# Optimization experiments

Measured on AMD Instinct MI355X. Metric: run time of the kernel, lower is better.

Reference implementation:

```python
import jax, jax.numpy as jnp
import numpy as np

CODE_DIM = 256
HIDDEN = 128
HEADS = 4
N_CODES = 100000
N_SPEC = 256


def setup_inputs() -> dict:
    key = jax.random.key(0)
    ks = jax.random.split(key, 7)
    provider_emb = jax.random.normal(ks[0], (CODE_DIM,), jnp.float32)
    code_embs = jax.random.normal(ks[1], (N_CODES, CODE_DIM), jnp.float32)
    # per-head Linear(code_dim -> hidden): stacked weights [H, D, K] and bias [H, K]
    W = jax.random.normal(ks[2], (HEADS, CODE_DIM, HIDDEN), jnp.float32) / np.sqrt(CODE_DIM)
    b = jax.random.normal(ks[3], (HEADS, HIDDEN), jnp.float32) * 0.01
    # attention vectors a: [H, 2*hidden] (squeezed trailing 1)
    a = jax.random.normal(ks[4], (HEADS, 2 * HIDDEN), jnp.float32) * 0.01
    # classifier Linear(hidden*heads -> num_specialties)
    Wc = jax.random.normal(ks[5], (N_SPEC, HIDDEN * HEADS), jnp.float32) / np.sqrt(HIDDEN * HEADS)
    bc = jax.random.normal(ks[6], (N_SPEC,), jnp.float32) * 0.01
    return {"provider_emb": provider_emb, "code_embs": code_embs,
            "W": W, "b": b, "a": a, "Wc": Wc, "bc": bc}


def reference(provider_emb, code_embs, W, b, a, Wc, bc):
    # provider projection per head: [H, K]
    provider_h = jnp.einsum('d,hdk->hk', provider_emb, W) + b
    # code projection per head: [H, N, K]
    code_h = jnp.einsum('nd,hdk->hnk', code_embs, W) + b[:, None, :]
    a1, a2 = a[:, :HIDDEN], a[:, HIDDEN:]           # split concat attention vec
    # e[h,n] = leaky_relu(provider_h[h].a1[h] + code_h[h,n].a2[h])
    e = jnp.einsum('hk,hk->h', provider_h, a1)[:, None] \
        + jnp.einsum('hnk,hk->hn', code_h, a2)
    e = jnp.where(e >= 0, e, 0.2 * e)               # LeakyReLU(0.2)
    alpha = jax.nn.softmax(e, axis=1)               # softmax over code nodes
    # dropout is identity in eval mode
    agg = jnp.einsum('hn,hnk->hk', alpha, code_h)   # weighted sum per head
    multi_head_output = agg.reshape(-1)             # [H*K]
    specialty_logits = multi_head_output @ Wc.T + bc
    return specialty_logits, multi_head_output
```

## Files before the change

kernel.cpp:

```cpp
#include <hip/hip_runtime.h>
#include <hip/hip_bf16.h>

#define CODE_DIM 256
#define HIDDEN   128
#define HEADS    4
#define N_CODES  100000
#define N_SPEC   256

#define K2_BLOCKS 1024
#define K2_TPB    256
#define K2_WPB    4
#define K2_WAVES  (K2_BLOCKS * K2_WPB)
#define WROWS     8
#define NTILES    (N_CODES / WROWS)
#define RSTRIDE   260
#define NSLOTS    64

#define WS_V       0
#define WS_CP      1024
#define WS_SLOT    1040
#define SLOT_STRIDE 1028

#define LDS_VSH   0
#define LDS_TSH   1024
#define LDS_TILE  1152
#define LDS_TOTAL (LDS_TILE + K2_WPB * WROWS * RSTRIDE)

#define WAITCNT_VM0   0x0F70
#define WAITCNT_LGKM0 0xC07F

typedef __attribute__((address_space(1))) const void* as1cv;
typedef __attribute__((address_space(3))) void*       as3v;

__global__ void k1_prep(const float* __restrict__ pe, const float* __restrict__ W,
                        const float* __restrict__ b, const float* __restrict__ a,
                        float* __restrict__ ws) {
    const int bx = blockIdx.x;
    const int h = bx >> 2, dq = bx & 3;
    const int tid = threadIdx.x;
    const int dl = tid >> 2, q = tid & 3;
    const int d = dq * 64 + dl;
    __shared__ float a_sh[2 * HIDDEN];
    __shared__ float cred[4];
    a_sh[tid] = a[h * 2 * HIDDEN + tid];
    __syncthreads();

    const float4* wr = (const float4*)(W + ((size_t)(h * CODE_DIM + d)) * HIDDEN + q * 32);
    float u = 0.f, v = 0.f;
#pragma unroll
    for (int j = 0; j < 8; ++j) {
        float4 wv = wr[j];
        int k = q * 32 + j * 4;
        u += wv.x * a_sh[k]     + wv.y * a_sh[k + 1]
           + wv.z * a_sh[k + 2] + wv.w * a_sh[k + 3];
        v += wv.x * a_sh[HIDDEN + k]     + wv.y * a_sh[HIDDEN + k + 1]
           + wv.z * a_sh[HIDDEN + k + 2] + wv.w * a_sh[HIDDEN + k + 3];
    }
    u += __shfl_xor(u, 1, 64); u += __shfl_xor(u, 2, 64);
    v += __shfl_xor(v, 1, 64); v += __shfl_xor(v, 2, 64);
    if (q == 0) ws[WS_V + h * CODE_DIM + d] = v;

    float cp = (q == 0) ? pe[d] * u : 0.f;
    if (dq == 0 && tid < HIDDEN) cp += b[h * HIDDEN + tid] * (a_sh[tid] + a_sh[HIDDEN + tid]);
#pragma unroll
    for (int off = 32; off; off >>= 1) cp += __shfl_xor(cp, off, 64);
    if ((tid & 63) == 0) cred[tid >> 6] = cp;
    __syncthreads();
    if (tid == 0) ws[WS_CP + h * 4 + dq] = cred[0] + cred[1] + cred[2] + cred[3];

    float4* z = (float4*)(ws + WS_SLOT);
    const int g = bx * 256 + tid;
#pragma unroll
    for (int i = 0; i < 5; ++i) {
        int idx = g + i * 4096;
        if (idx < (NSLOTS * SLOT_STRIDE) / 4) z[idx] = make_float4(0.f, 0.f, 0.f, 0.f);
    }
}

__global__ __launch_bounds__(K2_TPB, 4) void k2_main(const float* __restrict__ code,
                                                     float* __restrict__ ws) {
    __shared__ float lds[LDS_TOTAL];
    const int tid  = threadIdx.x;
    const int lane = tid & 63;
    const int w    = tid >> 6;
    const int row  = lane >> 3;
    const int seg  = lane & 7;
    const int bx   = blockIdx.x;

    {
        float4 vv = ((const float4*)(ws + WS_V))[tid];
        *(float4*)&lds[LDS_VSH + tid * 4] = vv;
    }
    float ch[HEADS];
#pragma unroll
    for (int h = 0; h < HEADS; ++h) {
        float4 cc = *(const float4*)(ws + WS_CP + 4 * h);
        ch[h] = cc.x + cc.y + cc.z + cc.w;
    }
    __syncthreads();

    const int tilebase = LDS_TILE + w * (WROWS * RSTRIDE);
    const int xb = tilebase + row * RSTRIDE + seg * 32;

    float4 acc0 = make_float4(0,0,0,0), acc1 = acc0, acc2 = acc0, acc3 = acc0;
    float ds0 = 0.f, ds1 = 0.f, ds2 = 0.f, ds3 = 0.f;

    for (int tile = bx * K2_WPB + w; tile < NTILES; tile += K2_WAVES) {
        __builtin_amdgcn_s_waitcnt(WAITCNT_LGKM0);
        const float* gbase = code + (size_t)tile * (WROWS * CODE_DIM) + lane * 4;
#pragma unroll
        for (int r = 0; r < WROWS; ++r) {
            __builtin_amdgcn_global_load_lds((as1cv)(gbase + r * CODE_DIM),
                                             (as3v)&lds[tilebase + r * RSTRIDE], 16, 0, 0);
        }
        __builtin_amdgcn_s_waitcnt(WAITCNT_VM0);

        float p0 = 0.f, p1 = 0.f, p2 = 0.f, p3 = 0.f;
#pragma unroll
        for (int c = 0; c < 8; ++c) {
            float4 x4 = *(const float4*)&lds[xb + c * 4];
            float4 va = *(const float4*)&lds[LDS_VSH +   0 + seg * 32 + c * 4];
            float4 vb = *(const float4*)&lds[LDS_VSH + 256 + seg * 32 + c * 4];
            float4 vc = *(const float4*)&lds[LDS_VSH + 512 + seg * 32 + c * 4];
            float4 vd = *(const float4*)&lds[LDS_VSH + 768 + seg * 32 + c * 4];
            p0 += x4.x * va.x + x4.y * va.y + x4.z * va.z + x4.w * va.w;
            p1 += x4.x * vb.x + x4.y * vb.y + x4.z * vb.z + x4.w * vb.w;
            p2 += x4.x * vc.x + x4.y * vc.y + x4.z * vc.z + x4.w * vc.w;
            p3 += x4.x * vd.x + x4.y * vd.y + x4.z * vd.z + x4.w * vd.w;
        }
#pragma unroll
        for (int off = 1; off < 8; off <<= 1) {
            p0 += __shfl_xor(p0, off, 64);
            p1 += __shfl_xor(p1, off, 64);
            p2 += __shfl_xor(p2, off, 64);
            p3 += __shfl_xor(p3, off, 64);
        }
        float e0 = p0 + ch[0]; e0 = (e0 >= 0.f) ? e0 : 0.2f * e0; float t0 = __expf(e0);
        float e1 = p1 + ch[1]; e1 = (e1 >= 0.f) ? e1 : 0.2f * e1; float t1 = __expf(e1);
        float e2 = p2 + ch[2]; e2 = (e2 >= 0.f) ? e2 : 0.2f * e2; float t2 = __expf(e2);
        float e3 = p3 + ch[3]; e3 = (e3 >= 0.f) ? e3 : 0.2f * e3; float t3 = __expf(e3);
        ds0 += t0; ds1 += t1; ds2 += t2; ds3 += t3;
        if (seg == 0) *(float4*)&lds[LDS_TSH + w * 32 + row * 4] = make_float4(t0, t1, t2, t3);
        __builtin_amdgcn_s_waitcnt(WAITCNT_LGKM0);

#pragma unroll
        for (int r = 0; r < WROWS; ++r) {
            float4 tr = *(const float4*)&lds[LDS_TSH + w * 32 + r * 4];
            float4 x4 = *(const float4*)&lds[tilebase + r * RSTRIDE + lane * 4];
            acc0.x += tr.x * x4.x; acc0.y += tr.x * x4.y; acc0.z += tr.x * x4.z; acc0.w += tr.x * x4.w;
            acc1.x += tr.y * x4.x; acc1.y += tr.y * x4.y; acc1.z += tr.y * x4.z; acc1.w += tr.y * x4.w;
            acc2.x += tr.z * x4.x; acc2.y += tr.z * x4.y; acc2.z += tr.z * x4.z; acc2.w += tr.z * x4.w;
            acc3.x += tr.w * x4.x; acc3.y += tr.w * x4.y; acc3.z += tr.w * x4.z; acc3.w += tr.w * x4.w;
        }
    }

    __syncthreads();
    *(float4*)&lds[w * 1024 +   0 + 4 * lane] = acc0;
    *(float4*)&lds[w * 1024 + 256 + 4 * lane] = acc1;
    *(float4*)&lds[w * 1024 + 512 + 4 * lane] = acc2;
    *(float4*)&lds[w * 1024 + 768 + 4 * lane] = acc3;
    *(float4*)&lds[4096 + (w * 64 + lane) * 4] = make_float4(ds0, ds1, ds2, ds3);
    __syncthreads();

    float* slot = ws + WS_SLOT + (size_t)(bx & (NSLOTS - 1)) * SLOT_STRIDE;
    for (int o = tid; o < HEADS * CODE_DIM; o += K2_TPB) {
        float s = lds[o] + lds[1024 + o] + lds[2048 + o] + lds[3072 + o];
        atomicAdd(slot + o, s);
    }
    {
        const int h = tid >> 6, l2 = tid & 63;
        float dv = lds[4096 +   0 + l2 * 4 + h] + lds[4096 + 256 + l2 * 4 + h]
                 + lds[4096 + 512 + l2 * 4 + h] + lds[4096 + 768 + l2 * 4 + h];
#pragma unroll
        for (int off = 32; off; off >>= 1) dv += __shfl_xor(dv, off, 64);
        if (l2 == 0) atomicAdd(slot + HEADS * CODE_DIM + h, dv * 0.125f);
    }
}

__global__ void k3_agg(const float* __restrict__ W, const float* __restrict__ b,
                       const float* __restrict__ ws, float* __restrict__ out) {
    const int bx = blockIdx.x;
    const int h = bx >> 2, q = bx & 3;
    const int tid = threadIdx.x;
    __shared__ float s_sh[CODE_DIM];
    __shared__ float yred[8 * 32];
    __shared__ float den_sh;
    const float* slots = ws + WS_SLOT;

    if (tid < 64) {
        float dv = slots[(size_t)tid * SLOT_STRIDE + HEADS * CODE_DIM + h];
#pragma unroll
        for (int off = 32; off; off >>= 1) dv += __shfl_xor(dv, off, 64);
        if (tid == 0) den_sh = dv;
    }
    float su = 0.f;
#pragma unroll 8
    for (int s2 = 0; s2 < NSLOTS; ++s2)
        su += slots[(size_t)s2 * SLOT_STRIDE + h * CODE_DIM + tid];
    __syncthreads();
    s_sh[tid] = su / den_sh;
    __syncthreads();

    const int c = tid >> 5, kl = tid & 31;
    float y = 0.f;
    const float* wp = W + ((size_t)(h * CODE_DIM + c * 32)) * HIDDEN + q * 32 + kl;
#pragma unroll 8
    for (int d = 0; d < 32; ++d) y += s_sh[c * 32 + d] * wp[(size_t)d * HIDDEN];
    yred[c * 32 + kl] = y;
    __syncthreads();
    if (tid < 32) {
        float t = 0.f;
#pragma unroll
        for (int cc = 0; cc < 8; ++cc) t += yred[cc * 32 + tid];
        out[N_SPEC + h * HIDDEN + q * 32 + tid] = t + b[h * HIDDEN + q * 32 + tid];
    }
}

__global__ void k4_logits(const float* __restrict__ Wc, const float* __restrict__ bc,
                          float* __restrict__ out) {
    const int lane = threadIdx.x & 63;
    const int wv   = threadIdx.x >> 6;
    const int i    = blockIdx.x * 4 + wv;
    const float4* wr  = (const float4*)(Wc + (size_t)i * (HEADS * HIDDEN));
    const float4* mh4 = (const float4*)(out + N_SPEC);
    float4 wa = wr[lane],      ma = mh4[lane];
    float4 wb = wr[64 + lane], mb = mh4[64 + lane];
    float pp = wa.x * ma.x + wa.y * ma.y + wa.z * ma.z + wa.w * ma.w
             + wb.x * mb.x + wb.y * mb.y + wb.z * mb.z + wb.w * mb.w;
#pragma unroll
    for (int off = 32; off; off >>= 1) pp += __shfl_xor(pp, off, 64);
    if (lane == 0) out[i] = pp + bc[i];
}

extern "C" void kernel_launch(void* const* d_in, const int* in_sizes, int n_in,
                              void* d_out, int out_size, void* d_ws, size_t ws_size,
                              hipStream_t stream) {
    const float* pe   = (const float*)d_in[0];
    const float* code = (const float*)d_in[1];
    const float* W    = (const float*)d_in[2];
    const float* b    = (const float*)d_in[3];
    const float* a    = (const float*)d_in[4];
    const float* Wc   = (const float*)d_in[5];
    const float* bc   = (const float*)d_in[6];
    float* out = (float*)d_out;
    float* ws  = (float*)d_ws;

    k1_prep<<<16, 256, 0, stream>>>(pe, W, b, a, ws);
    k2_main<<<K2_BLOCKS, K2_TPB, 0, stream>>>(code, ws);
    k3_agg<<<16, 256, 0, stream>>>(W, b, ws, out);
    k4_logits<<<64, 256, 0, stream>>>(Wc, bc, out);
}
```

Measured before the change: 177.9 us.

## Use atomic work-stealing tile counter in main kernel and widen prep grid

Result: slower. 334.0 us (+87.7%).

```diff
diff --git a/kernel.cpp b/kernel.cpp
--- a/kernel.cpp
+++ b/kernel.cpp
@@ -10,7 +10,6 @@
 #define K2_BLOCKS 1024
 #define K2_TPB    256
 #define K2_WPB    4
-#define K2_WAVES  (K2_BLOCKS * K2_WPB)
 #define WROWS     8
 #define NTILES    (N_CODES / WROWS)
 #define RSTRIDE   260
@@ -18,7 +17,8 @@
 
 #define WS_V       0
 #define WS_CP      1024
-#define WS_SLOT    1040
+#define WS_CTR     1088
+#define WS_SLOT    1104
 #define SLOT_STRIDE 1028
 
 #define LDS_VSH   0
@@ -36,50 +36,54 @@
                         const float* __restrict__ b, const float* __restrict__ a,
                         float* __restrict__ ws) {
     const int bx = blockIdx.x;
-    const int h = bx >> 2, dq = bx & 3;
+    const int h = bx >> 4, dseg = bx & 15;
     const int tid = threadIdx.x;
-    const int dl = tid >> 2, q = tid & 3;
-    const int d = dq * 64 + dl;
+    const int dl = tid >> 4;
+    const int q  = tid & 15;
+    const int d  = dseg * 16 + dl;
     __shared__ float a_sh[2 * HIDDEN];
     __shared__ float cred[4];
     a_sh[tid] = a[h * 2 * HIDDEN + tid];
     __syncthreads();
 
-    const float4* wr = (const float4*)(W + ((size_t)(h * CODE_DIM + d)) * HIDDEN + q * 32);
+    const float4* wr = (const float4*)(W + ((size_t)(h * CODE_DIM + d)) * HIDDEN + q * 8);
     float u = 0.f, v = 0.f;
 #pragma unroll
-    for (int j = 0; j < 8; ++j) {
+    for (int j = 0; j < 2; ++j) {
         float4 wv = wr[j];
-        int k = q * 32 + j * 4;
+        int k = q * 8 + j * 4;
         u += wv.x * a_sh[k]     + wv.y * a_sh[k + 1]
            + wv.z * a_sh[k + 2] + wv.w * a_sh[k + 3];
         v += wv.x * a_sh[HIDDEN + k]     + wv.y * a_sh[HIDDEN + k + 1]
            + wv.z * a_sh[HIDDEN + k + 2] + wv.w * a_sh[HIDDEN + k + 3];
     }
-    u += __shfl_xor(u, 1, 64); u += __shfl_xor(u, 2, 64);
-    v += __shfl_xor(v, 1, 64); v += __shfl_xor(v, 2, 64);
+#pragma unroll
+    for (int off = 1; off < 16; off <<= 1) {
+        u += __shfl_xor(u, off, 64);
+        v += __shfl_xor(v, off, 64);
+    }
     if (q == 0) ws[WS_V + h * CODE_DIM + d] = v;
 
     float cp = (q == 0) ? pe[d] * u : 0.f;
-    if (dq == 0 && tid < HIDDEN) cp += b[h * HIDDEN + tid] * (a_sh[tid] + a_sh[HIDDEN + tid]);
+    if (dseg == 0 && tid < HIDDEN) cp += b[h * HIDDEN + tid] * (a_sh[tid] + a_sh[HIDDEN + tid]);
 #pragma unroll
     for (int off = 32; off; off >>= 1) cp += __shfl_xor(cp, off, 64);
     if ((tid & 63) == 0) cred[tid >> 6] = cp;
     __syncthreads();
-    if (tid == 0) ws[WS_CP + h * 4 + dq] = cred[0] + cred[1] + cred[2] + cred[3];
+    if (tid == 0) ws[WS_CP + bx] = cred[0] + cred[1] + cred[2] + cred[3];
+    if (bx == 0 && tid == 0) *(int*)(ws + WS_CTR) = 0;
 
     float4* z = (float4*)(ws + WS_SLOT);
     const int g = bx * 256 + tid;
-#pragma unroll
-    for (int i = 0; i < 5; ++i) {
-        int idx = g + i * 4096;
-        if (idx < (NSLOTS * SLOT_STRIDE) / 4) z[idx] = make_float4(0.f, 0.f, 0.f, 0.f);
-    }
+    const int nz = (NSLOTS * SLOT_STRIDE) / 4;
+    z[g] = make_float4(0.f, 0.f, 0.f, 0.f);
+    if (g + 16384 < nz) z[g + 16384] = make_float4(0.f, 0.f, 0.f, 0.f);
 }
 
 __global__ __launch_bounds__(K2_TPB, 4) void k2_main(const float* __restrict__ code,
                                                      float* __restrict__ ws) {
     __shared__ float lds[LDS_TOTAL];
+    __shared__ float c_sh[HEADS];
     const int tid  = threadIdx.x;
     const int lane = tid & 63;
     const int w    = tid >> 6;
@@ -91,21 +95,30 @@
         float4 vv = ((const float4*)(ws + WS_V))[tid];
         *(float4*)&lds[LDS_VSH + tid * 4] = vv;
     }
+    if (tid < 64) {
+        float cpv = ws[WS_CP + tid];
+#pragma unroll
+        for (int off = 1; off < 16; off <<= 1) cpv += __shfl_xor(cpv, off, 64);
+        if ((tid & 15) == 0) c_sh[tid >> 4] = cpv;
+    }
+    __syncthreads();
     float ch[HEADS];
 #pragma unroll
-    for (int h = 0; h < HEADS; ++h) {
-        float4 cc = *(const float4*)(ws + WS_CP + 4 * h);
-        ch[h] = cc.x + cc.y + cc.z + cc.w;
-    }
-    __syncthreads();
+    for (int h = 0; h < HEADS; ++h) ch[h] = c_sh[h];
 
     const int tilebase = LDS_TILE + w * (WROWS * RSTRIDE);
     const int xb = tilebase + row * RSTRIDE + seg * 32;
+    int* ctr = (int*)(ws + WS_CTR);
 
     float4 acc0 = make_float4(0,0,0,0), acc1 = acc0, acc2 = acc0, acc3 = acc0;
     float ds0 = 0.f, ds1 = 0.f, ds2 = 0.f, ds3 = 0.f;
 
-    for (int tile = bx * K2_WPB + w; tile < NTILES; tile += K2_WAVES) {
+    for (;;) {
+        int tile;
+        if (lane == 0) tile = atomicAdd(ctr, 1);
+        tile = __shfl(tile, 0, 64);
+        if (tile >= NTILES) break;
+
         __builtin_amdgcn_s_waitcnt(WAITCNT_LGKM0);
         const float* gbase = code + (size_t)tile * (WROWS * CODE_DIM) + lane * 4;
 #pragma unroll
@@ -245,7 +258,7 @@
     float* out = (float*)d_out;
     float* ws  = (float*)d_ws;
 
-    k1_prep<<<16, 256, 0, stream>>>(pe, W, b, a, ws);
+    k1_prep<<<64, 256, 0, stream>>>(pe, W, b, a, ws);
     k2_main<<<K2_BLOCKS, K2_TPB, 0, stream>>>(code, ws);
     k3_agg<<<16, 256, 0, stream>>>(W, b, ws, out);
     k4_logits<<<64, 256, 0, stream>>>(Wc, bc, out);
```
